# Performance work log

Measured on AMD Instinct MI355X. Metric: run time of the kernel, lower is better.

## Reference

```python
import jax, jax.numpy as jnp
import numpy as np

INPUT_SIZE = 1024
HIDDEN_SIZE = 1024
B, L = 32, 2048


def setup_inputs() -> dict:
    key = jax.random.key(0)
    k_h, k_m, k_lw, k_vw, k_vq = jax.random.split(key, 5)
    h = jax.random.normal(k_h, (B, L, INPUT_SIZE), dtype=jnp.float32)
    mask = jax.random.randint(k_m, (B, L), 0, 2).astype(bool)
    # nn.Linear(input+hidden, hidden): weight (hidden, input+hidden), bias (hidden,)
    fan = INPUT_SIZE + HIDDEN_SIZE + HIDDEN_SIZE
    ln_w = jax.random.uniform(k_lw, (HIDDEN_SIZE, INPUT_SIZE + HIDDEN_SIZE),
                              minval=-1.0, maxval=1.0, dtype=jnp.float32) * np.sqrt(6.0 / fan)
    ln_b = jnp.zeros((HIDDEN_SIZE,), dtype=jnp.float32)
    # v: Linear(hidden, 1, bias=False) -> weight (1, hidden); store as (hidden,)
    v_w = jax.random.uniform(k_vw, (HIDDEN_SIZE,), minval=-1.0, maxval=1.0,
                             dtype=jnp.float32) * np.sqrt(6.0 / (HIDDEN_SIZE + 1))
    vq = jax.random.uniform(k_vq, (HIDDEN_SIZE,), dtype=jnp.float32)
    return {"h": h, "mask": mask, "ln_w": ln_w, "ln_b": ln_b, "v_w": v_w, "vq": vq}


def reference(h, mask, ln_w, ln_b, v_w, vq):
    # ln(cat([h, vq], -1)) == h @ W_h^T + vq @ W_vq^T + b  (vq is constant over b,l)
    W_h = ln_w[:, :INPUT_SIZE]          # (H, I)
    W_vq = ln_w[:, INPUT_SIZE:]         # (H, H)
    bias = ln_b + W_vq @ vq             # (H,)
    pre = jnp.einsum('bli,hi->blh', h, W_h) + bias  # (B, L, H)
    s = jnp.tanh(pre) @ v_w             # (B, L)
    s = s - (~mask).astype(s.dtype) * 10000.0
    a = jax.nn.softmax(s, axis=1)       # softmax over seq dim
    r = jnp.einsum('bl,bli->bi', a, h)  # (B, I)
    return r  # dropout omitted (eval mode)
```

## Files before the change

kernel.cpp:

```cpp
#include <hip/hip_runtime.h>
#include <hip/hip_bf16.h>

typedef short  bf16x8s __attribute__((ext_vector_type(8)));
typedef float  f32x4   __attribute__((ext_vector_type(4)));

#define BATCH 32
#define SEQL  2048
#define NROWS (BATCH * SEQL)
#define IN    1024
#define HID   1024

#define WHB_OFF   0u
#define BIAS_OFF  0x200000u
#define SPART_OFF 0x210000u
#define ABUF_OFF  0x610000u
#define HB_OFF    0x650000u
#define RPART_OFF SPART_OFF
#define WS_NEED_BF16 ((size_t)HB_OFF + (size_t)NROWS * IN * 2)

__device__ __forceinline__ unsigned int pack2bf(float f0, float f1) {
    unsigned int u0 = __float_as_uint(f0) + 0x8000u;
    unsigned int u1 = __float_as_uint(f1) + 0x8000u;
    return __builtin_amdgcn_perm(u1, u0, 0x07060302u);
}

__device__ __forceinline__ float tanh_fast(float x) {
    float xc = fminf(fmaxf(x, -15.f), 15.f);
    float t  = __builtin_amdgcn_exp2f(xc * 2.8853900817779268f);
    return (t - 1.f) * __builtin_amdgcn_rcpf(t + 1.f);
}

__device__ __forceinline__ void gl2lds16(const void* g, void* l) {
    __builtin_amdgcn_global_load_lds(
        (const __attribute__((address_space(1))) unsigned int*)g,
        (__attribute__((address_space(3))) unsigned int*)l, 16, 0, 0);
}

__device__ __forceinline__ void block_map(int bi, int& rb, int& cb) {
    int xcd  = bi & 7;
    int slot = bi >> 3;
    rb = xcd + 8 * (slot >> 3);
    cb = slot & 7;
}

__global__ __launch_bounds__(256) void prep_kernel(const float* __restrict__ ln_w,
                                                   const float* __restrict__ ln_b,
                                                   const float* __restrict__ vq,
                                                   const float* __restrict__ h,
                                                   unsigned short* __restrict__ whb,
                                                   float* __restrict__ bias,
                                                   unsigned short* __restrict__ hb) {
    const int bi = blockIdx.x;
    const int t  = threadIdx.x;
    if (bi < 1024) {
        const int n = bi;
        const int wave = t >> 6;
        const int lane = t & 63;
        float4 v = ((const float4*)(ln_w + (size_t)n * 2048))[t];
        uint2 pk;
        pk.x = pack2bf(v.x, v.y);
        pk.y = pack2bf(v.z, v.w);
        *(uint2*)(whb + (size_t)n * 1024 + t * 4) = pk;
        const float* wrow = ln_w + (size_t)n * 2048 + 1024;
        float s = 0.f;
        #pragma unroll
        for (int j = 0; j < 4; ++j) {
            int k = t + j * 256;
            s += wrow[k] * vq[k];
        }
        #pragma unroll
        for (int off = 32; off; off >>= 1) s += __shfl_xor(s, off);
        __shared__ float red[4];
        if (lane == 0) red[wave] = s;
        __syncthreads();
        if (t == 0) bias[n] = ln_b[n] + red[0] + red[1] + red[2] + red[3];
    } else {
        size_t idx = ((size_t)(bi - 1024) * 256 + t) * 8;
        float4 a = *(const float4*)(h + idx);
        float4 b = *(const float4*)(h + idx + 4);
        uint4 p;
        p.x = pack2bf(a.x, a.y); p.y = pack2bf(a.z, a.w);
        p.z = pack2bf(b.x, b.y); p.w = pack2bf(b.z, b.w);
        *(uint4*)(hb + idx) = p;
    }
}

__global__ __launch_bounds__(512) void gemm256_kernel(const unsigned short* __restrict__ hb,
                                                      const unsigned short* __restrict__ whb,
                                                      const float* __restrict__ bias,
                                                      const float* __restrict__ vw,
                                                      float* __restrict__ s_part) {
    __shared__ __align__(16) unsigned short As[8192];
    __shared__ __align__(16) unsigned short Bs[4096];

    const int tid = threadIdx.x;
    int rb, cb;
    block_map(blockIdx.x, rb, cb);
    const int wave = tid >> 6;
    const int lane = tid & 63;
    const int quad = lane >> 4;
    const int l15  = lane & 15;
    const int wy   = wave >> 1;
    const int wx   = wave & 1;
    const int row0 = rb * 256;
    const int col0 = cb * 128;

    const int srow = tid >> 2;
    const int sg   = tid & 3;
    const int swz  = (srow >> 1) & 3;
    const unsigned short* gA0 = hb  + (size_t)(row0 + srow) * 1024 + ((sg ^ swz) * 8);
    const unsigned short* gA1 = gA0 + (size_t)128 * 1024;
    const unsigned short* gB0 = whb + (size_t)(col0 + srow) * 1024 + ((sg ^ swz) * 8);
    unsigned short* lA0 = As + tid * 8;
    unsigned short* lA1 = As + 4096 + tid * 8;
    unsigned short* lB0 = Bs + tid * 8;

    const unsigned short* rA[4];
    const unsigned short* rB[4];
    #pragma unroll
    for (int i = 0; i < 4; ++i) {
        int ra = wy * 64 + i * 16 + l15;
        rA[i] = As + ra * 32 + ((quad ^ ((ra >> 1) & 3)) * 8);
        int rn = wx * 64 + i * 16 + l15;
        rB[i] = Bs + rn * 32 + ((quad ^ ((rn >> 1) & 3)) * 8);
    }

    f32x4 acc[4][4];
    #pragma unroll
    for (int i = 0; i < 4; ++i)
        #pragma unroll
        for (int j = 0; j < 4; ++j)
            acc[i][j] = (f32x4){0.f, 0.f, 0.f, 0.f};

    for (int k0 = 0; k0 < 1024; k0 += 32) {
        __syncthreads();
        gl2lds16(gA0 + k0, lA0);
        gl2lds16(gA1 + k0, lA1);
        gl2lds16(gB0 + k0, lB0);
        __syncthreads();

        bf16x8s af[4], bfv[4];
        #pragma unroll
        for (int i = 0; i < 4; ++i) af[i]  = *(const bf16x8s*)rA[i];
        #pragma unroll
        for (int i = 0; i < 4; ++i) bfv[i] = *(const bf16x8s*)rB[i];
        #pragma unroll
        for (int mt = 0; mt < 4; ++mt)
            #pragma unroll
            for (int nt = 0; nt < 4; ++nt)
                acc[mt][nt] = __builtin_amdgcn_mfma_f32_16x16x32_bf16(af[mt], bfv[nt], acc[mt][nt], 0, 0, 0);
    }

    const int colb = col0 + wx * 64 + l15;
    float vwv[4], bv[4];
    #pragma unroll
    for (int nt = 0; nt < 4; ++nt) {
        vwv[nt] = vw[colb + nt * 16];
        bv[nt]  = bias[colb + nt * 16];
    }
    const int rowb = row0 + wy * 64 + quad * 4;
    const int colp = cb * 2 + wx;
    #pragma unroll
    for (int mt = 0; mt < 4; ++mt) {
        #pragma unroll
        for (int r = 0; r < 4; ++r) {
            float p = 0.f;
            #pragma unroll
            for (int nt = 0; nt < 4; ++nt)
                p += tanh_fast(acc[mt][nt][r] + bv[nt]) * vwv[nt];
            p += __shfl_xor(p, 1);
            p += __shfl_xor(p, 2);
            p += __shfl_xor(p, 4);
            p += __shfl_xor(p, 8);
            if (l15 == 0) s_part[(size_t)(rowb + mt * 16 + r) * 16 + colp] = p;
        }
    }
}

__global__ __launch_bounds__(256) void gemm_f32_kernel(const float* __restrict__ hmat,
                                                       const unsigned short* __restrict__ whb,
                                                       const float* __restrict__ bias,
                                                       const float* __restrict__ vw,
                                                       float* __restrict__ s_part) {
    __shared__ __align__(16) unsigned short As[4096];
    __shared__ __align__(16) unsigned short Bs[4096];
    const int tid = threadIdx.x;
    int rb, cb;
    block_map(blockIdx.x, rb, cb);
    const int wave = tid >> 6;
    const int lane = tid & 63;
    const int quad = lane >> 4;
    const int l15  = lane & 15;
    const int wy   = wave >> 1;
    const int wx   = wave & 1;
    const int row0 = rb * 128;
    const int col0 = cb * 128;
    const int srow = tid >> 2;
    const int sg   = tid & 3;
    const int swz  = (srow >> 1) & 3;
    const float*          gA0 = hmat + (size_t)(row0 + srow)      * 1024 + sg * 8;
    const float*          gA1 = hmat + (size_t)(row0 + srow + 64) * 1024 + sg * 8;
    const unsigned short* gB0 = whb  + (size_t)(col0 + srow)      * 1024 + ((sg ^ swz) * 8);
    unsigned short* wA0 = As + srow * 32 + ((sg ^ swz) * 8);
    unsigned short* wA1 = wA0 + 64 * 32;
    unsigned short* lB0 = Bs + tid * 8;
    const unsigned short* rA[4];
    const unsigned short* rB[4];
    #pragma unroll
    for (int i = 0; i < 4; ++i) {
        int ra = wy * 64 + i * 16 + l15;
        rA[i] = As + ra * 32 + ((quad ^ ((ra >> 1) & 3)) * 8);
        int rn = wx * 64 + i * 16 + l15;
        rB[i] = Bs + rn * 32 + ((quad ^ ((rn >> 1) & 3)) * 8);
    }
    f32x4 acc[4][4];
    #pragma unroll
    for (int i = 0; i < 4; ++i)
        #pragma unroll
        for (int j = 0; j < 4; ++j)
            acc[i][j] = (f32x4){0.f, 0.f, 0.f, 0.f};
    for (int k0 = 0; k0 < 1024; k0 += 32) {
        float4 va0 = *(const float4*)(gA0 + k0);
        float4 va1 = *(const float4*)(gA0 + k0 + 4);
        float4 va2 = *(const float4*)(gA1 + k0);
        float4 va3 = *(const float4*)(gA1 + k0 + 4);
        __syncthreads();
        gl2lds16(gB0 + k0, lB0);
        gl2lds16(gB0 + 65536 + k0, lB0 + 2048);
        uint4 pa0, pa1;
        pa0.x = pack2bf(va0.x, va0.y); pa0.y = pack2bf(va0.z, va0.w);
        pa0.z = pack2bf(va1.x, va1.y); pa0.w = pack2bf(va1.z, va1.w);
        pa1.x = pack2bf(va2.x, va2.y); pa1.y = pack2bf(va2.z, va2.w);
        pa1.z = pack2bf(va3.x, va3.y); pa1.w = pack2bf(va3.z, va3.w);
        *(uint4*)wA0 = pa0;
        *(uint4*)wA1 = pa1;
        __syncthreads();
        bf16x8s af[4], bfv[4];
        #pragma unroll
        for (int i = 0; i < 4; ++i) af[i]  = *(const bf16x8s*)rA[i];
        #pragma unroll
        for (int i = 0; i < 4; ++i) bfv[i] = *(const bf16x8s*)rB[i];
        #pragma unroll
        for (int mt = 0; mt < 4; ++mt)
            #pragma unroll
            for (int nt = 0; nt < 4; ++nt)
                acc[mt][nt] = __builtin_amdgcn_mfma_f32_16x16x32_bf16(af[mt], bfv[nt], acc[mt][nt], 0, 0, 0);
    }
    const int colb = col0 + wx * 64 + l15;
    float vwv[4], bv[4];
    #pragma unroll
    for (int nt = 0; nt < 4; ++nt) {
        vwv[nt] = vw[colb + nt * 16];
        bv[nt]  = bias[colb + nt * 16];
    }
    const int rowb = row0 + wy * 64 + quad * 4;
    const int colp = cb * 2 + wx;
    #pragma unroll
    for (int mt = 0; mt < 4; ++mt) {
        #pragma unroll
        for (int r = 0; r < 4; ++r) {
            float p = 0.f;
            #pragma unroll
            for (int nt = 0; nt < 4; ++nt)
                p += tanh_fast(acc[mt][nt][r] + bv[nt]) * vwv[nt];
            p += __shfl_xor(p, 1);
            p += __shfl_xor(p, 2);
            p += __shfl_xor(p, 4);
            p += __shfl_xor(p, 8);
            if (l15 == 0) s_part[(size_t)(rowb + mt * 16 + r) * 16 + colp] = p;
        }
    }
}

__global__ __launch_bounds__(512) void softmax_kernel(const float* __restrict__ s_part,
                                                      const int* __restrict__ mask,
                                                      float* __restrict__ a_buf) {
    const int b    = blockIdx.x;
    const int t    = threadIdx.x;
    const int wave = t >> 6;
    const int lane = t & 63;
    __shared__ float redm[8];
    __shared__ float reds[8];
    float sv[4];
    float mx = -3.0e38f;
    #pragma unroll
    for (int j = 0; j < 4; ++j) {
        int l = t + j * 512;
        const float4* pr = (const float4*)(s_part + ((size_t)b * 2048 + l) * 16);
        float4 q0 = pr[0], q1 = pr[1], q2 = pr[2], q3 = pr[3];
        float v = (q0.x + q0.y + q0.z + q0.w) + (q1.x + q1.y + q1.z + q1.w)
                + (q2.x + q2.y + q2.z + q2.w) + (q3.x + q3.y + q3.z + q3.w);
        if (mask[b * 2048 + l] == 0) v -= 10000.f;
        sv[j] = v;
        mx = fmaxf(mx, v);
    }
    #pragma unroll
    for (int off = 32; off; off >>= 1) mx = fmaxf(mx, __shfl_xor(mx, off));
    if (lane == 0) redm[wave] = mx;
    __syncthreads();
    mx = redm[0];
    #pragma unroll
    for (int w = 1; w < 8; ++w) mx = fmaxf(mx, redm[w]);
    float sum = 0.f;
    #pragma unroll
    for (int j = 0; j < 4; ++j) {
        sv[j] = __expf(sv[j] - mx);
        sum += sv[j];
    }
    #pragma unroll
    for (int off = 32; off; off >>= 1) sum += __shfl_xor(sum, off);
    if (lane == 0) reds[wave] = sum;
    __syncthreads();
    sum = reds[0];
    #pragma unroll
    for (int w = 1; w < 8; ++w) sum += reds[w];
    float inv = 1.f / sum;
    #pragma unroll
    for (int j = 0; j < 4; ++j)
        a_buf[b * 2048 + t + j * 512] = sv[j] * inv;
}

__global__ __launch_bounds__(256) void r_bf16_part_kernel(const unsigned short* __restrict__ hb,
                                                          const float* __restrict__ a_buf,
                                                          float* __restrict__ r_part) {
    const int b  = blockIdx.x >> 5;
    const int lc = blockIdx.x & 31;
    const int t  = threadIdx.x;
    __shared__ float aw[64];
    if (t < 64) aw[t] = a_buf[b * 2048 + lc * 64 + t];
    __syncthreads();
    const uint2* hp = (const uint2*)(hb + (size_t)(b * 2048 + lc * 64) * 1024) + t;
    float a0 = 0.f, a1 = 0.f, a2 = 0.f, a3 = 0.f;
    #pragma unroll 8
    for (int l = 0; l < 64; ++l) {
        uint2 v = hp[(size_t)l * 256];
        float av = aw[l];
        a0 += av * __uint_as_float(v.x << 16);
        a1 += av * __uint_as_float(v.x & 0xffff0000u);
        a2 += av * __uint_as_float(v.y << 16);
        a3 += av * __uint_as_float(v.y & 0xffff0000u);
    }
    float4 res = {a0, a1, a2, a3};
    *(float4*)(r_part + ((size_t)lc * 32 + b) * 1024 + t * 4) = res;
}

__global__ __launch_bounds__(256) void r_f32_part_kernel(const float* __restrict__ hmat,
                                                         const float* __restrict__ a_buf,
                                                         float* __restrict__ r_part) {
    const int b  = blockIdx.x >> 5;
    const int lc = blockIdx.x & 31;
    const int t  = threadIdx.x;
    __shared__ float aw[64];
    if (t < 64) aw[t] = a_buf[b * 2048 + lc * 64 + t];
    __syncthreads();
    const float4* hp = (const float4*)hmat + (size_t)(b * 2048 + lc * 64) * 256;
    float ax = 0.f, ay = 0.f, az = 0.f, aq = 0.f;
    #pragma unroll 8
    for (int l = 0; l < 64; ++l) {
        float4 hv = hp[(size_t)l * 256 + t];
        float av = aw[l];
        ax += av * hv.x; ay += av * hv.y; az += av * hv.z; aq += av * hv.w;
    }
    float4 res = {ax, ay, az, aq};
    *(float4*)(r_part + ((size_t)lc * 32 + b) * 1024 + t * 4) = res;
}

__global__ __launch_bounds__(256) void r_reduce_kernel(const float* __restrict__ r_part,
                                                       float* __restrict__ out) {
    const int b = blockIdx.x;
    const int t = threadIdx.x;
    float4 s = {0.f, 0.f, 0.f, 0.f};
    #pragma unroll 8
    for (int lc = 0; lc < 32; ++lc) {
        float4 v = *(const float4*)(r_part + ((size_t)lc * 32 + b) * 1024 + t * 4);
        s.x += v.x; s.y += v.y; s.z += v.z; s.w += v.w;
    }
    *(float4*)(out + b * 1024 + t * 4) = s;
}

extern "C" void kernel_launch(void* const* d_in, const int* in_sizes, int n_in,
                              void* d_out, int out_size, void* d_ws, size_t ws_size,
                              hipStream_t stream) {
    const float* h    = (const float*)d_in[0];
    const int*   mask = (const int*)d_in[1];
    const float* ln_w = (const float*)d_in[2];
    const float* ln_b = (const float*)d_in[3];
    const float* v_w  = (const float*)d_in[4];
    const float* vq   = (const float*)d_in[5];
    float* out = (float*)d_out;

    char* ws = (char*)d_ws;
    unsigned short* whb = (unsigned short*)(ws + WHB_OFF);
    float* bias         = (float*)(ws + BIAS_OFF);
    float* s_part       = (float*)(ws + SPART_OFF);
    float* a_buf        = (float*)(ws + ABUF_OFF);
    unsigned short* hb  = (unsigned short*)(ws + HB_OFF);
    float* r_part       = (float*)(ws + RPART_OFF);

    const bool use_bf16_h = (ws_size >= WS_NEED_BF16);

    if (use_bf16_h) {
        prep_kernel<<<1024 + 32768, 256, 0, stream>>>(ln_w, ln_b, vq, h, whb, bias, hb);
        gemm256_kernel<<<(NROWS / 256) * (HID / 128), 512, 0, stream>>>(hb, whb, bias, v_w, s_part);
        softmax_kernel<<<BATCH, 512, 0, stream>>>(s_part, mask, a_buf);
        r_bf16_part_kernel<<<BATCH * 32, 256, 0, stream>>>(hb, a_buf, r_part);
        r_reduce_kernel<<<BATCH, 256, 0, stream>>>(r_part, out);
    } else {
        prep_kernel<<<1024, 256, 0, stream>>>(ln_w, ln_b, vq, h, whb, bias, hb);
        gemm_f32_kernel<<<(NROWS / 128) * (HID / 128), 256, 0, stream>>>(h, whb, bias, v_w, s_part);
        softmax_kernel<<<BATCH, 512, 0, stream>>>(s_part, mask, a_buf);
        r_f32_part_kernel<<<BATCH * 32, 256, 0, stream>>>(h, a_buf, r_part);
        r_reduce_kernel<<<BATCH, 256, 0, stream>>>(r_part, out);
    }
}
```

Measured before the change: 554.4 us.

## Fuse softmax with weighted sum and drop partial-reduction pass

Merges the softmax, attention-weighted sum and final reduction into one kernel per (batch, 128-column chunk). Each workgroup recomputes the softmax for its batch row, keeps the weights in LDS, and reduces across waves in LDS before writing the output directly. This removes two launches and the a_buf and r_part round trips through global memory. In exchange the softmax is done redundantly 8 times per batch, and only 256 workgroups read hb with 4-byte-per-lane accesses, which could lower memory parallelism.

```diff
diff --git a/kernel.cpp b/kernel.cpp
--- a/kernel.cpp
+++ b/kernel.cpp
@@ -13,9 +13,7 @@
 #define WHB_OFF   0u
 #define BIAS_OFF  0x200000u
 #define SPART_OFF 0x210000u
-#define ABUF_OFF  0x610000u
 #define HB_OFF    0x650000u
-#define RPART_OFF SPART_OFF
 #define WS_NEED_BF16 ((size_t)HB_OFF + (size_t)NROWS * IN * 2)
 
 __device__ __forceinline__ unsigned int pack2bf(float f0, float f1) {
@@ -272,15 +270,22 @@
     }
 }
 
-__global__ __launch_bounds__(512) void softmax_kernel(const float* __restrict__ s_part,
-                                                      const int* __restrict__ mask,
-                                                      float* __restrict__ a_buf) {
-    const int b    = blockIdx.x;
+__global__ __launch_bounds__(512) void fused_sm_r_bf16(const float* __restrict__ s_part,
+                                                       const int* __restrict__ mask,
+                                                       const unsigned short* __restrict__ hb,
+                                                       float* __restrict__ out) {
+    const int wg   = blockIdx.x;
+    const int b    = wg & 31;
+    const int cc   = wg >> 5;
     const int t    = threadIdx.x;
-    const int wave = t >> 6;
+    const int w    = t >> 6;
     const int lane = t & 63;
+
+    __shared__ float a_lds[2048];
+    __shared__ float red[8][128];
     __shared__ float redm[8];
     __shared__ float reds[8];
+
     float sv[4];
     float mx = -3.0e38f;
     #pragma unroll
@@ -296,86 +301,129 @@
     }
     #pragma unroll
     for (int off = 32; off; off >>= 1) mx = fmaxf(mx, __shfl_xor(mx, off));
-    if (lane == 0) redm[wave] = mx;
+    if (lane == 0) redm[w] = mx;
     __syncthreads();
     mx = redm[0];
     #pragma unroll
-    for (int w = 1; w < 8; ++w) mx = fmaxf(mx, redm[w]);
+    for (int i = 1; i < 8; ++i) mx = fmaxf(mx, redm[i]);
     float sum = 0.f;
     #pragma unroll
     for (int j = 0; j < 4; ++j) {
-        sv[j] = __expf(sv[j] - mx);
-        sum += sv[j];
+        float e = __expf(sv[j] - mx);
+        a_lds[t + j * 512] = e;
+        sum += e;
     }
     #pragma unroll
     for (int off = 32; off; off >>= 1) sum += __shfl_xor(sum, off);
-    if (lane == 0) reds[wave] = sum;
+    if (lane == 0) reds[w] = sum;
     __syncthreads();
     sum = reds[0];
     #pragma unroll
-    for (int w = 1; w < 8; ++w) sum += reds[w];
-    float inv = 1.f / sum;
+    for (int i = 1; i < 8; ++i) sum += reds[i];
+    const float inv = 1.f / sum;
     #pragma unroll
     for (int j = 0; j < 4; ++j)
-        a_buf[b * 2048 + t + j * 512] = sv[j] * inv;
-}
-
-__global__ __launch_bounds__(256) void r_bf16_part_kernel(const unsigned short* __restrict__ hb,
-                                                          const float* __restrict__ a_buf,
-                                                          float* __restrict__ r_part) {
-    const int b  = blockIdx.x >> 5;
-    const int lc = blockIdx.x & 31;
-    const int t  = threadIdx.x;
-    __shared__ float aw[64];
-    if (t < 64) aw[t] = a_buf[b * 2048 + lc * 64 + t];
-    __syncthreads();
-    const uint2* hp = (const uint2*)(hb + (size_t)(b * 2048 + lc * 64) * 1024) + t;
-    float a0 = 0.f, a1 = 0.f, a2 = 0.f, a3 = 0.f;
+        a_lds[t + j * 512] *= inv;
+    __syncthreads();
+
+    const unsigned int* hp = (const unsigned int*)
+        (hb + (size_t)b * 2048 * 1024 + cc * 128 + lane * 2);
+    float acc0 = 0.f, acc1 = 0.f;
     #pragma unroll 8
-    for (int l = 0; l < 64; ++l) {
-        uint2 v = hp[(size_t)l * 256];
-        float av = aw[l];
-        a0 += av * __uint_as_float(v.x << 16);
-        a1 += av * __uint_as_float(v.x & 0xffff0000u);
-        a2 += av * __uint_as_float(v.y << 16);
-        a3 += av * __uint_as_float(v.y & 0xffff0000u);
-    }
-    float4 res = {a0, a1, a2, a3};
-    *(float4*)(r_part + ((size_t)lc * 32 + b) * 1024 + t * 4) = res;
-}
-
-__global__ __launch_bounds__(256) void r_f32_part_kernel(const float* __restrict__ hmat,
-                                                         const float* __restrict__ a_buf,
-                                                         float* __restrict__ r_part) {
-    const int b  = blockIdx.x >> 5;
-    const int lc = blockIdx.x & 31;
-    const int t  = threadIdx.x;
-    __shared__ float aw[64];
-    if (t < 64) aw[t] = a_buf[b * 2048 + lc * 64 + t];
-    __syncthreads();
-    const float4* hp = (const float4*)hmat + (size_t)(b * 2048 + lc * 64) * 256;
-    float ax = 0.f, ay = 0.f, az = 0.f, aq = 0.f;
+    for (int i = 0; i < 256; ++i) {
+        const int l = w + i * 8;
+        unsigned int v = hp[(size_t)l * 512];
+        float av = a_lds[l];
+        acc0 += av * __uint_as_float(v << 16);
+        acc1 += av * __uint_as_float(v & 0xffff0000u);
+    }
+    red[w][lane * 2]     = acc0;
+    red[w][lane * 2 + 1] = acc1;
+    __syncthreads();
+    if (t < 128) {
+        float s = 0.f;
+        #pragma unroll
+        for (int i = 0; i < 8; ++i) s += red[i][t];
+        out[b * 1024 + cc * 128 + t] = s;
+    }
+}
+
+__global__ __launch_bounds__(512) void fused_sm_r_f32(const float* __restrict__ s_part,
+                                                      const int* __restrict__ mask,
+                                                      const float* __restrict__ hmat,
+                                                      float* __restrict__ out) {
+    const int wg   = blockIdx.x;
+    const int b    = wg & 31;
+    const int cc   = wg >> 5;
+    const int t    = threadIdx.x;
+    const int w    = t >> 6;
+    const int lane = t & 63;
+
+    __shared__ float a_lds[2048];
+    __shared__ float red[8][128];
+    __shared__ float redm[8];
+    __shared__ float reds[8];
+
+    float sv[4];
+    float mx = -3.0e38f;
+    #pragma unroll
+    for (int j = 0; j < 4; ++j) {
+        int l = t + j * 512;
+        const float4* pr = (const float4*)(s_part + ((size_t)b * 2048 + l) * 16);
+        float4 q0 = pr[0], q1 = pr[1], q2 = pr[2], q3 = pr[3];
+        float v = (q0.x + q0.y + q0.z + q0.w) + (q1.x + q1.y + q1.z + q1.w)
+                + (q2.x + q2.y + q2.z + q2.w) + (q3.x + q3.y + q3.z + q3.w);
+        if (mask[b * 2048 + l] == 0) v -= 10000.f;
+        sv[j] = v;
+        mx = fmaxf(mx, v);
+    }
+    #pragma unroll
+    for (int off = 32; off; off >>= 1) mx = fmaxf(mx, __shfl_xor(mx, off));
+    if (lane == 0) redm[w] = mx;
+    __syncthreads();
+    mx = redm[0];
+    #pragma unroll
+    for (int i = 1; i < 8; ++i) mx = fmaxf(mx, redm[i]);
+    float sum = 0.f;
+    #pragma unroll
+    for (int j = 0; j < 4; ++j) {
+        float e = __expf(sv[j] - mx);
+        a_lds[t + j * 512] = e;
+        sum += e;
+    }
+    #pragma unroll
+    for (int off = 32; off; off >>= 1) sum += __shfl_xor(sum, off);
+    if (lane == 0) reds[w] = sum;
+    __syncthreads();
+    sum = reds[0];
+    #pragma unroll
+    for (int i = 1; i < 8; ++i) sum += reds[i];
+    const float inv = 1.f / sum;
+    #pragma unroll
+    for (int j = 0; j < 4; ++j)
+        a_lds[t + j * 512] *= inv;
+    __syncthreads();
+
+    const float2* hp = (const float2*)
+        (hmat + (size_t)b * 2048 * 1024 + cc * 128 + lane * 2);
+    float acc0 = 0.f, acc1 = 0.f;
     #pragma unroll 8
-    for (int l = 0; l < 64; ++l) {
-        float4 hv = hp[(size_t)l * 256 + t];
-        float av = aw[l];
-        ax += av * hv.x; ay += av * hv.y; az += av * hv.z; aq += av * hv.w;
-    }
-    float4 res = {ax, ay, az, aq};
-    *(float4*)(r_part + ((size_t)lc * 32 + b) * 1024 + t * 4) = res;
-}
-
-__global__ __launch_bounds__(256) void r_reduce_kernel(const float* __restrict__ r_part,
-                                                       float* __restrict__ out) {
-    const int b = blockIdx.x;
-    const int t = threadIdx.x;
-    float4 s = {0.f, 0.f, 0.f, 0.f};
-    #pragma unroll 8
-    for (int lc = 0; lc < 32; ++lc) {
-        float4 v = *(const float4*)(r_part + ((size_t)lc * 32 + b) * 1024 + t * 4);
-        s.x += v.x; s.y += v.y; s.z += v.z; s.w += v.w;
-    }
-    *(float4*)(out + b * 1024 + t * 4) = s;
+    for (int i = 0; i < 256; ++i) {
+        const int l = w + i * 8;
+        float2 v = hp[(size_t)l * 512];
+        float av = a_lds[l];
+        acc0 += av * v.x;
+        acc1 += av * v.y;
+    }
+    red[w][lane * 2]     = acc0;
+    red[w][lane * 2 + 1] = acc1;
+    __syncthreads();
+    if (t < 128) {
+        float s = 0.f;
+        #pragma unroll
+        for (int i = 0; i < 8; ++i) s += red[i][t];
+        out[b * 1024 + cc * 128 + t] = s;
+    }
 }
 
 extern "C" void kernel_launch(void* const* d_in, const int* in_sizes, int n_in,
@@ -393,23 +441,17 @@
     unsigned short* whb = (unsigned short*)(ws + WHB_OFF);
     float* bias         = (float*)(ws + BIAS_OFF);
     float* s_part       = (float*)(ws + SPART_OFF);
-    float* a_buf        = (float*)(ws + ABUF_OFF);
     unsigned short* hb  = (unsigned short*)(ws + HB_OFF);
-    float* r_part       = (float*)(ws + RPART_OFF);
 
     const bool use_bf16_h = (ws_size >= WS_NEED_BF16);
 
     if (use_bf16_h) {
         prep_kernel<<<1024 + 32768, 256, 0, stream>>>(ln_w, ln_b, vq, h, whb, bias, hb);
         gemm256_kernel<<<(NROWS / 256) * (HID / 128), 512, 0, stream>>>(hb, whb, bias, v_w, s_part);
-        softmax_kernel<<<BATCH, 512, 0, stream>>>(s_part, mask, a_buf);
-        r_bf16_part_kernel<<<BATCH * 32, 256, 0, stream>>>(hb, a_buf, r_part);
-        r_reduce_kernel<<<BATCH, 256, 0, stream>>>(r_part, out);
+        fused_sm_r_bf16<<<256, 512, 0, stream>>>(s_part, mask, hb, out);
     } else {
         prep_kernel<<<1024, 256, 0, stream>>>(ln_w, ln_b, vq, h, whb, bias, hb);
         gemm_f32_kernel<<<(NROWS / 128) * (HID / 128), 256, 0, stream>>>(h, whb, bias, v_w, s_part);
-        softmax_kernel<<<BATCH, 512, 0, stream>>>(s_part, mask, a_buf);
-        r_f32_part_kernel<<<BATCH * 32, 256, 0, stream>>>(h, a_buf, r_part);
-        r_reduce_kernel<<<BATCH, 256, 0, stream>>>(r_part, out);
-    }
-}
+        fused_sm_r_f32<<<256, 512, 0, stream>>>(s_part, mask, h, out);
+    }
+}
```

Result: no change. 548.2 us (-1.1%).
